# Performance work log

Hardware: AMD Instinct MI355X
Metric: run time of the kernel (lower is better)

Reference implementation:

```python
import jax, jax.numpy as jnp
import numpy as np

VAR0, VAR1 = 0.1, 0.2
THRESH = 0.5
NEG_POS = 3
NEG_INF = -1e30


def point_form(b):
    # (cx,cy,w,h) -> (x1,y1,x2,y2)
    return jnp.concatenate([b[..., :2] - b[..., 2:] * 0.5,
                            b[..., :2] + b[..., 2:] * 0.5], -1)


def iou(a, b):
    # a: [G,4], b: [A,4], both xyxy -> [G,A]
    tl = jnp.maximum(a[:, None, :2], b[None, :, :2])
    br = jnp.minimum(a[:, None, 2:], b[None, :, 2:])
    wh = jnp.clip(br - tl, 0.0)
    inter = wh[..., 0] * wh[..., 1]
    area_a = (a[:, 2] - a[:, 0]) * (a[:, 3] - a[:, 1])
    area_b = (b[:, 2] - b[:, 0]) * (b[:, 3] - b[:, 1])
    return inter / (area_a[:, None] + area_b[None, :] - inter)


def encode_single(gt_boxes, gt_labels, anchors):
    # gt_boxes [G,4] xyxy, gt_labels [G], anchors [A,4] cxcywh
    ov = iou(gt_boxes, point_form(anchors))            # [G,A]
    best_prior_idx = jnp.argmax(ov, axis=1)            # [G] guaranteed match
    best_truth_ov = jnp.max(ov, axis=0)                # [A]
    best_truth_idx = jnp.argmax(ov, axis=0)            # [A]
    G = gt_boxes.shape[0]
    best_truth_ov = best_truth_ov.at[best_prior_idx].set(2.0)
    best_truth_idx = best_truth_idx.at[best_prior_idx].set(jnp.arange(G))
    matches = gt_boxes[best_truth_idx]                 # [A,4]
    conf = jnp.where(best_truth_ov < THRESH, 0, gt_labels[best_truth_idx] + 1)
    m_cxcy = (matches[:, :2] + matches[:, 2:]) * 0.5
    m_wh = matches[:, 2:] - matches[:, :2]
    g_cxcy = (m_cxcy - anchors[:, :2]) / (VAR0 * anchors[:, 2:])
    g_wh = jnp.log(m_wh / anchors[:, 2:]) / VAR1
    return conf, jnp.concatenate([g_cxcy, g_wh], -1)


def smooth_l1(d):
    ad = jnp.abs(d)
    return jnp.where(ad < 1.0, 0.5 * d * d, ad - 0.5)


def ssd_guarantee_loss(pred_conf, pred_loc, anchors_b, gt_boxes, gt_labels):
    # anchors_b: per-image anchors [B,A,4] (cxcywh)
    conf_t, loc_t = jax.vmap(encode_single)(gt_boxes, gt_labels, anchors_b)
    loc_t = jax.lax.stop_gradient(loc_t)               # loc_t.detach() in torch
    pos = conf_t > 0                                   # [B,A]
    N = jnp.sum(pos).astype(pred_loc.dtype)
    loc_loss = jnp.sum(jnp.where(pos[..., None], smooth_l1(pred_loc - loc_t), 0.0))
    logp = jax.nn.log_softmax(pred_conf, axis=-1)
    ce = -jnp.take_along_axis(logp, conf_t[..., None], axis=-1)[..., 0]  # [B,A]
    A = pred_conf.shape[1]
    pos_num = jnp.sum(pos, axis=1)                     # [B]
    neg_num = jnp.maximum(10, jnp.minimum(pos_num * NEG_POS, A - pos_num))
    neg_ce = jnp.where(conf_t == 0, ce, NEG_INF)
    neg_sorted = -jnp.sort(-neg_ce, axis=1)            # descending hard-negative sort
    rank = jnp.arange(A)
    take = (rank[None, :] < neg_num[:, None]) & (neg_sorted > 0.5 * NEG_INF)
    class_loss = (jnp.sum(jnp.where(pos, ce, 0.0))
                  + jnp.sum(jnp.where(take, neg_sorted, 0.0))) / N
    return class_loss, loc_loss / N, N


def decode(loc, anchors):
    # loc [B,A,4], anchors [A,4] cxcywh -> refined anchors [B,A,4] cxcywh
    cxcy = anchors[None, :, :2] + loc[..., :2] * VAR0 * anchors[None, :, 2:]
    wh = anchors[None, :, 2:] * jnp.exp(loc[..., 2:] * VAR1)
    return jnp.concatenate([cxcy, wh], -1)


def setup_inputs() -> dict:
    key = jax.random.key(0)
    ks = jax.random.split(key, 10)
    B, A, C, G = 32, 16320, 81, 32
    objectness = jax.random.normal(ks[0], (B, A, 2), jnp.float32)
    refine_loc = 0.1 * jax.random.normal(ks[1], (B, A, 4), jnp.float32)
    pred_conf = jax.random.normal(ks[2], (B, A, C), jnp.float32)
    pred_loc = 0.1 * jax.random.normal(ks[3], (B, A, 4), jnp.float32)
    # anchors: valid normalized cxcywh
    a_cxcy = 0.05 + 0.9 * jax.random.uniform(ks[4], (1, A, 2), jnp.float32)
    a_wh = 0.02 + 0.23 * jax.random.uniform(ks[5], (1, A, 2), jnp.float32)
    anchors = jnp.concatenate([a_cxcy, a_wh], -1)
    # gt boxes: valid xyxy in [0,1]
    g_cxcy = 0.2 + 0.6 * jax.random.uniform(ks[6], (B, G, 2), jnp.float32)
    g_wh = 0.05 + 0.25 * jax.random.uniform(ks[7], (B, G, 2), jnp.float32)
    gt_boxes = jnp.clip(jnp.concatenate([g_cxcy - g_wh * 0.5, g_cxcy + g_wh * 0.5], -1), 0.0, 1.0)
    gt_labels = jax.random.randint(ks[8], (B, G), 0, C - 1, jnp.int32)
    return {"objectness": objectness, "refine_loc": refine_loc, "pred_conf": pred_conf,
            "pred_loc": pred_loc, "anchors": anchors, "gt_boxes": gt_boxes,
            "gt_labels": gt_labels}


def reference(objectness, refine_loc, pred_conf, pred_loc, anchors, gt_boxes, gt_labels):
    a0 = anchors[0]                                    # [A,4]
    B = pred_conf.shape[0]
    anchors_b = jnp.broadcast_to(a0, (B,) + a0.shape)
    # ARM: binary objectness, labels zeroed
    arm_cls, arm_loc, _ = ssd_guarantee_loss(objectness, refine_loc, anchors_b,
                                             gt_boxes, jnp.zeros_like(gt_labels))
    # ODM: match against per-image refined anchors
    refined = decode(refine_loc, a0)
    odm_cls, odm_loc, _ = ssd_guarantee_loss(pred_conf, pred_loc, refined,
                                             gt_boxes, gt_labels)
    total = arm_cls + arm_loc + odm_cls + odm_loc
    return (total, odm_cls, odm_loc, arm_cls, arm_loc)
```

## Files before the change

### kernel.cpp

```cpp
#include <hip/hip_runtime.h>
#include <hip/hip_bf16.h>

constexpr int NB = 32;
constexpr int NA = 16320;
constexpr int NG = 32;
constexpr int NC = 81;
constexpr int ODM_GRID = 2048;

__device__ __forceinline__ float sl1(float d) {
    float ad = fabsf(d);
    return ad < 1.f ? 0.5f * d * d : ad - 0.5f;
}

__device__ __forceinline__ unsigned long long umax64(unsigned long long a, unsigned long long b) {
    return a > b ? a : b;
}

__global__ __launch_bounds__(256) void k_match(
    const float* __restrict__ anchors,
    const float* __restrict__ refine_loc,
    const float* __restrict__ gt_boxes,
    float* __restrict__ ws_ov,
    unsigned char* __restrict__ ws_idx,
    unsigned long long* __restrict__ ws_part)
{
    int row = blockIdx.x >> 6;
    int chunk = blockIdx.x & 63;
    int lossId = row >> 5, b = row & 31;
    int tid = threadIdx.x;
    __shared__ float4 s_gt[NG];
    __shared__ float s_ga[NG];
    __shared__ unsigned long long s_part[4][NG];
    if (tid < NG) {
        float4 g = *(const float4*)&gt_boxes[(size_t)(b * NG + tid) * 4];
        s_gt[tid] = g;
        s_ga[tid] = (g.z - g.x) * (g.w - g.y);
    }
    __syncthreads();
    int a = chunk * 256 + tid;
    bool valid = a < NA;
    int al = valid ? a : NA - 1;
    float4 an = *(const float4*)&anchors[(size_t)al * 4];
    float acx = an.x, acy = an.y, aw = an.z, ah = an.w;
    if (lossId) {
        float4 rl = *(const float4*)&refine_loc[((size_t)b * NA + al) * 4];
        acx += rl.x * 0.1f * aw;
        acy += rl.y * 0.1f * ah;
        aw *= __expf(rl.z * 0.2f);
        ah *= __expf(rl.w * 0.2f);
    }
    float ax1 = acx - aw * 0.5f, ay1 = acy - ah * 0.5f;
    float ax2 = acx + aw * 0.5f, ay2 = acy + ah * 0.5f;
    float aarea = (ax2 - ax1) * (ay2 - ay1);

    float ovg[NG];
    float best = -1.f; int bg = 0;
    #pragma unroll
    for (int g = 0; g < NG; g++) {
        float4 G = s_gt[g];
        float tlx = fmaxf(G.x, ax1);
        float tly = fmaxf(G.y, ay1);
        float brx = fminf(G.z, ax2);
        float bry = fminf(G.w, ay2);
        float w = brx - tlx; w = w > 0.f ? w : 0.f;
        float h = bry - tly; h = h > 0.f ? h : 0.f;
        float inter = w * h;
        float uni = s_ga[g] + aarea - inter;
        float ov = inter * __builtin_amdgcn_rcpf(uni);
        if (!valid) ov = 0.f;
        ovg[g] = ov;
        if (ov > best) { best = ov; bg = g; }
    }
    if (valid) {
        size_t sec = (size_t)row * NA;
        ws_ov[sec + a] = best;
        ws_idx[sec + a] = (unsigned char)bg;
    }
    int lane = tid & 63, wv = tid >> 6;
    #pragma unroll
    for (int g = 0; g < NG; g++) {
        float m = ovg[g];
        m = fmaxf(m, __shfl_xor(m, 1));
        m = fmaxf(m, __shfl_xor(m, 2));
        m = fmaxf(m, __shfl_xor(m, 4));
        m = fmaxf(m, __shfl_xor(m, 8));
        m = fmaxf(m, __shfl_xor(m, 16));
        m = fmaxf(m, __shfl_xor(m, 32));
        unsigned long long ball = __ballot(ovg[g] == m);
        int first = __ffsll((long long)ball) - 1;
        if (lane == 0) {
            unsigned aw_ = (unsigned)(chunk * 256 + wv * 64 + first);
            s_part[wv][g] = ((unsigned long long)__float_as_uint(m) << 32)
                            | (0xFFFFFFFFu - aw_);
        }
    }
    __syncthreads();
    if (tid < NG) {
        unsigned long long k = s_part[0][tid];
        #pragma unroll
        for (int i = 1; i < 4; i++) k = umax64(k, s_part[i][tid]);
        ws_part[(size_t)blockIdx.x * NG + tid] = k;
    }
}

__global__ __launch_bounds__(256) void k_conf(
    const int* __restrict__ gt_labels,
    const unsigned long long* __restrict__ ws_part,
    const float* __restrict__ ws_ov,
    const unsigned char* __restrict__ ws_idx,
    const float* __restrict__ objectness,
    const float* __restrict__ anchors,
    const float* __restrict__ gt_boxes,
    const float* __restrict__ arm_pred,
    int* __restrict__ match,
    float* __restrict__ negce,
    int* __restrict__ pos_cnt,
    float2* __restrict__ pConf)
{
    int row = blockIdx.x >> 3;
    int chunk = blockIdx.x & 7;
    int lossId = row >> 5, b = row & 31;
    int tid = threadIdx.x;
    __shared__ int s_oa[NG];
    __shared__ int s_lab[NG];
    __shared__ float4 s_gt[NG];
    __shared__ unsigned s_mask[512];
    __shared__ unsigned long long s_pp[8][NG];
    for (int i = tid; i < 512; i += 256) s_mask[i] = 0u;
    {
        int g = tid & 31, s = tid >> 5;
        unsigned long long k = 0ull;
        for (int c = s; c < 64; c += 8)
            k = umax64(k, ws_part[(size_t)(row * 64 + c) * NG + g]);
        s_pp[s][g] = k;
    }
    __syncthreads();
    if (tid < NG) {
        unsigned long long k = s_pp[0][tid];
        #pragma unroll
        for (int i = 1; i < 8; i++) k = umax64(k, s_pp[i][tid]);
        unsigned a = 0xFFFFFFFFu - (unsigned)(k & 0xFFFFFFFFull);
        s_oa[tid] = (int)a;
        s_lab[tid] = lossId ? gt_labels[b * NG + tid] : 0;
        s_gt[tid] = *(const float4*)&gt_boxes[(size_t)(b * NG + tid) * 4];
        atomicOr(&s_mask[a >> 5], 1u << (a & 31));
    }
    __syncthreads();
    size_t sec = (size_t)row * NA;
    int base = chunk * 2040;
    int cnt = 0;
    float pce = 0.f, ploc = 0.f;
    for (int a = base + tid; a < base + 2040; a += 256) {
        float ov = ws_ov[sec + a];
        int g = ws_idx[sec + a];
        if (s_mask[a >> 5] & (1u << (a & 31))) {
            for (int j = NG - 1; j >= 0; j--)
                if (s_oa[j] == a) { g = j; ov = 2.0f; break; }
        }
        int conf = (ov < 0.5f) ? 0 : (s_lab[g] + 1);
        cnt += (conf > 0);
        if (lossId) {
            match[sec + a] = conf | (g << 16);
        } else {
            size_t idx = sec + a;
            float2 x = *(const float2*)&objectness[idx * 2];
            float lse = __logf(__expf(x.x) + __expf(x.y));
            float ce = lse - (conf ? x.y : x.x);
            if (conf > 0) {
                pce += ce;
                negce[idx] = 0.f;
                float4 an = *(const float4*)&anchors[(size_t)a * 4];
                float4 G = s_gt[g];
                float mcx = (G.x + G.z) * 0.5f, mcy = (G.y + G.w) * 0.5f;
                float mw = G.z - G.x, mh = G.w - G.y;
                float t0 = (mcx - an.x) / (0.1f * an.z);
                float t1 = (mcy - an.y) / (0.1f * an.w);
                float t2 = __logf(mw / an.z) / 0.2f;
                float t3 = __logf(mh / an.w) / 0.2f;
                float4 pl = *(const float4*)&arm_pred[idx * 4];
                ploc += sl1(pl.x - t0) + sl1(pl.y - t1) + sl1(pl.z - t2) + sl1(pl.w - t3);
            } else {
                negce[idx] = ce;
            }
        }
    }
    #pragma unroll
    for (int o = 32; o > 0; o >>= 1) {
        cnt += __shfl_down(cnt, o);
        pce += __shfl_down(pce, o);
        ploc += __shfl_down(ploc, o);
    }
    __shared__ int s_c[4];
    __shared__ float s_p0[4], s_p1[4];
    if ((tid & 63) == 0) {
        int w = tid >> 6;
        s_c[w] = cnt; s_p0[w] = pce; s_p1[w] = ploc;
    }
    __syncthreads();
    if (tid == 0) {
        pos_cnt[blockIdx.x] = s_c[0] + s_c[1] + s_c[2] + s_c[3];
        pConf[blockIdx.x] = make_float2(s_p0[0] + s_p0[1] + s_p0[2] + s_p0[3],
                                        s_p1[0] + s_p1[1] + s_p1[2] + s_p1[3]);
    }
}

__device__ __forceinline__ void block_reduce2_store(float v0, float v1, float2* dst) {
    #pragma unroll
    for (int o = 32; o > 0; o >>= 1) { v0 += __shfl_down(v0, o); v1 += __shfl_down(v1, o); }
    __shared__ float s0[4], s1[4];
    int w = threadIdx.x >> 6;
    if ((threadIdx.x & 63) == 0) { s0[w] = v0; s1[w] = v1; }
    __syncthreads();
    if (threadIdx.x == 0) {
        float t0 = 0.f, t1 = 0.f;
        #pragma unroll
        for (int i = 0; i < 4; i++) { t0 += s0[i]; t1 += s1[i]; }
        *dst = make_float2(t0, t1);
    }
}

__device__ __forceinline__ void odm_anchor(
    int idx, const float* x, float x80, int m, int sub,
    const float* __restrict__ anchors, const float* __restrict__ refine_loc,
    const float* __restrict__ gt_boxes, const float* __restrict__ pred_loc,
    float* __restrict__ negce, float& pce, float& ploc)
{
    int conf = m & 0xFFFF; int g = m >> 16;
    float s = (sub == 0) ? __expf(x80) : 0.f;
    float sel = (sub == 0 && conf == 80) ? x80 : 0.f;
    #pragma unroll
    for (int j = 0; j < 10; j++) {
        s += __expf(x[j]);
        sel += (sub + 8 * j == conf) ? x[j] : 0.f;
    }
    s += __shfl_xor(s, 1);   sel += __shfl_xor(sel, 1);
    s += __shfl_xor(s, 2);   sel += __shfl_xor(sel, 2);
    s += __shfl_xor(s, 4);   sel += __shfl_xor(sel, 4);
    float ce = __logf(s) - sel;
    if (sub == 0) {
        if (conf > 0) {
            pce += ce;
            negce[idx] = 0.f;
            int b = idx / NA, a = idx - b * NA;
            float4 an = *(const float4*)&anchors[(size_t)a * 4];
            float4 rl = *(const float4*)&refine_loc[(size_t)idx * 4];
            float acx = an.x + rl.x * 0.1f * an.z;
            float acy = an.y + rl.y * 0.1f * an.w;
            float aw = an.z * __expf(rl.z * 0.2f);
            float ah = an.w * __expf(rl.w * 0.2f);
            const float* gb = &gt_boxes[(size_t)(b * NG + g) * 4];
            float mcx = (gb[0] + gb[2]) * 0.5f, mcy = (gb[1] + gb[3]) * 0.5f;
            float mw = gb[2] - gb[0], mh = gb[3] - gb[1];
            float t0 = (mcx - acx) / (0.1f * aw);
            float t1 = (mcy - acy) / (0.1f * ah);
            float t2 = __logf(mw / aw) / 0.2f;
            float t3 = __logf(mh / ah) / 0.2f;
            float4 pl = *(const float4*)&pred_loc[(size_t)idx * 4];
            ploc += sl1(pl.x - t0) + sl1(pl.y - t1) + sl1(pl.z - t2) + sl1(pl.w - t3);
        } else {
            negce[idx] = ce;
        }
    }
}

__global__ __launch_bounds__(256, 4) void k_odm_loss(
    const float* __restrict__ pred_conf,
    const float* __restrict__ pred_loc,
    const float* __restrict__ anchors,
    const float* __restrict__ refine_loc,
    const float* __restrict__ gt_boxes,
    const int* __restrict__ match,
    float* __restrict__ negce,
    float2* __restrict__ partial)
{
    int lane = threadIdx.x & 63;
    int sub = lane & 7;
    int grp = lane >> 3;
    int wid = blockIdx.x * 4 + (threadIdx.x >> 6);
    const int NWAVE = ODM_GRID * 4;
    const int TOT = NB * NA / 8;
    float pce = 0.f, ploc = 0.f;

    float x[10], x80; int m, idx;
    {
        idx = wid * 8 + grp;
        const float* p = pred_conf + (size_t)idx * NC;
        #pragma unroll
        for (int j = 0; j < 10; j++) x[j] = p[sub + 8 * j];
        x80 = (sub == 0) ? p[80] : -87.f;
        m = match[idx];
    }
    for (int gi = wid; gi < TOT; gi += NWAVE) {
        float y[10], y80 = -87.f; int my = 0, idxy = 0;
        int nx = gi + NWAVE;
        if (nx < TOT) {
            idxy = nx * 8 + grp;
            const float* p = pred_conf + (size_t)idxy * NC;
            #pragma unroll
            for (int j = 0; j < 10; j++) y[j] = p[sub + 8 * j];
            y80 = (sub == 0) ? p[80] : -87.f;
            my = match[idxy];
        }
        odm_anchor(idx, x, x80, m, sub, anchors, refine_loc, gt_boxes, pred_loc,
                   negce, pce, ploc);
        #pragma unroll
        for (int j = 0; j < 10; j++) x[j] = y[j];
        x80 = y80; m = my; idx = idxy;
    }
    block_reduce2_store(pce, ploc, &partial[blockIdx.x]);
}

__global__ __launch_bounds__(512) void k_topk(
    const float* __restrict__ negce,
    const int* __restrict__ pos_cnt,
    float* __restrict__ topk)
{
    int blk = blockIdx.x;
    int tid = threadIdx.x;
    size_t sec = (size_t)blk * NA;
    float v[32];
    #pragma unroll
    for (int q = 0; q < 32; q++) {
        int i = tid + (q << 9);
        v[q] = (i < NA) ? negce[sec + i] : 0.f;
    }
    __shared__ int s_red[8];
    __shared__ float s_redf[8];
    int p = 0;
    #pragma unroll
    for (int j = 0; j < 8; j++) p += pos_cnt[blk * 8 + j];
    int k = p * 3; if (k > NA - p) k = NA - p; if (k < 10) k = 10;

    unsigned lo = 0u, hi = 0x7F800000u;
    while (lo < hi) {
        unsigned mid = (lo + hi) >> 1;
        float fmid = __uint_as_float(mid);
        int c = 0;
        #pragma unroll
        for (int q = 0; q < 32; q++) c += (v[q] > fmid);
        #pragma unroll
        for (int o = 32; o > 0; o >>= 1) c += __shfl_down(c, o);
        if ((tid & 63) == 0) s_red[tid >> 6] = c;
        __syncthreads();
        int total = 0;
        #pragma unroll
        for (int j = 0; j < 8; j++) total += s_red[j];
        __syncthreads();
        if (total < k) hi = mid; else lo = mid + 1;
    }
    float V = __uint_as_float(lo);
    int c = 0; float sum = 0.f;
    #pragma unroll
    for (int q = 0; q < 32; q++) {
        if (v[q] > V) { c++; sum += v[q]; }
    }
    #pragma unroll
    for (int o = 32; o > 0; o >>= 1) { c += __shfl_down(c, o); sum += __shfl_down(sum, o); }
    if ((tid & 63) == 0) { s_red[tid >> 6] = c; s_redf[tid >> 6] = sum; }
    __syncthreads();
    if (tid == 0) {
        int cg = 0; float sg = 0.f;
        #pragma unroll
        for (int j = 0; j < 8; j++) { cg += s_red[j]; sg += s_redf[j]; }
        topk[blk] = sg + (float)(k - cg) * V;
    }
}

__global__ __launch_bounds__(256) void k_final(
    const float2* __restrict__ pConf, const float2* __restrict__ pOdm,
    const int* __restrict__ pos_cnt, const float* __restrict__ topk,
    float* __restrict__ out)
{
    int tid = threadIdx.x;
    float a0 = 0.f, a1 = 0.f, o0 = 0.f, o1 = 0.f;
    for (int i = tid; i < 512; i += 256) { float2 v = pConf[i]; a0 += v.x; a1 += v.y; }
    for (int i = tid; i < ODM_GRID; i += 256) { float2 v = pOdm[i]; o0 += v.x; o1 += v.y; }
    float n0 = (float)pos_cnt[tid];
    float n1 = (float)pos_cnt[256 + tid];
    float t0 = (tid < NB) ? topk[tid] : 0.f;
    float t1 = (tid < NB) ? topk[NB + tid] : 0.f;
    #pragma unroll
    for (int o = 32; o > 0; o >>= 1) {
        a0 += __shfl_down(a0, o); a1 += __shfl_down(a1, o);
        o0 += __shfl_down(o0, o); o1 += __shfl_down(o1, o);
        n0 += __shfl_down(n0, o); n1 += __shfl_down(n1, o);
        t0 += __shfl_down(t0, o); t1 += __shfl_down(t1, o);
    }
    __shared__ float s[4][8];
    if ((tid & 63) == 0) {
        int w = tid >> 6;
        s[w][0] = a0; s[w][1] = a1; s[w][2] = o0; s[w][3] = o1;
        s[w][4] = n0; s[w][5] = n1; s[w][6] = t0; s[w][7] = t1;
    }
    __syncthreads();
    if (tid == 0) {
        float armce = 0.f, armloc = 0.f, odmce = 0.f, odmloc = 0.f;
        float N0 = 0.f, N1 = 0.f, tk0 = 0.f, tk1 = 0.f;
        #pragma unroll
        for (int i = 0; i < 4; i++) {
            armce += s[i][0]; armloc += s[i][1]; odmce += s[i][2]; odmloc += s[i][3];
            N0 += s[i][4]; N1 += s[i][5]; tk0 += s[i][6]; tk1 += s[i][7];
        }
        float cls0 = (armce + tk0) / N0, loc0 = armloc / N0;
        float cls1 = (odmce + tk1) / N1, loc1 = odmloc / N1;
        out[0] = cls0 + loc0 + cls1 + loc1;
        out[1] = cls1;
        out[2] = loc1;
        out[3] = cls0;
        out[4] = loc0;
    }
}

extern "C" void kernel_launch(void* const* d_in, const int* in_sizes, int n_in,
                              void* d_out, int out_size, void* d_ws, size_t ws_size,
                              hipStream_t stream) {
    const float* objectness = (const float*)d_in[0];
    const float* refine_loc = (const float*)d_in[1];
    const float* pred_conf  = (const float*)d_in[2];
    const float* pred_loc   = (const float*)d_in[3];
    const float* anchors    = (const float*)d_in[4];
    const float* gt_boxes   = (const float*)d_in[5];
    const int*   gt_labels  = (const int*)d_in[6];

    char* w = (char*)d_ws;
    size_t off = 0;
    int* pos_cnt = (int*)(w + off); off += 512 * sizeof(int);
    float* topk = (float*)(w + off); off += 64 * sizeof(float);
    off = (off + 15) & ~(size_t)15;
    float2* pConf = (float2*)(w + off); off += 512 * 8;
    float2* pOdm = (float2*)(w + off); off += (size_t)ODM_GRID * 8;
    unsigned long long* ws_part = (unsigned long long*)(w + off);
    off += (size_t)64 * 64 * NG * 8;
    off = (off + 15) & ~(size_t)15;
    float* ws_ov = (float*)(w + off); off += (size_t)2 * NB * NA * 4;
    unsigned char* ws_idx = (unsigned char*)(w + off); off += (size_t)2 * NB * NA;
    off = (off + 15) & ~(size_t)15;
    int* match = (int*)(w + off); off += (size_t)2 * NB * NA * 4;
    float* negce = (float*)(w + off); off += (size_t)2 * NB * NA * 4;

    k_match<<<64 * 64, 256, 0, stream>>>(anchors, refine_loc, gt_boxes,
                                         ws_ov, ws_idx, ws_part);
    k_conf<<<64 * 8, 256, 0, stream>>>(gt_labels, ws_part, ws_ov, ws_idx,
                                       objectness, anchors, gt_boxes, refine_loc,
                                       match, negce, pos_cnt, pConf);
    k_odm_loss<<<ODM_GRID, 256, 0, stream>>>(pred_conf, pred_loc, anchors, refine_loc,
                                             gt_boxes, match + (size_t)NB * NA,
                                             negce + (size_t)NB * NA, pOdm);
    k_topk<<<2 * NB, 512, 0, stream>>>(negce, pos_cnt, topk);
    k_final<<<1, 256, 0, stream>>>(pConf, pOdm, pos_cnt, topk, (float*)d_out);
}
```

Measured before the change: 131.1 us.

## Restructure pipeline into match+LSE mega kernel, fixup pass, and per-row loss kernel

Merges the IoU matching and the ODM log-sum-exp pass over pred_conf into one interleaved launch, so the memory-bound LSE streaming overlaps with the compute-bound matching. Confidence is computed directly during matching, and a small per-row fixup kernel applies the forced best-prior matches instead of rescanning every anchor. Per-row CE, localisation loss and top-k hard-negative mining are fused into one 1024-thread kernel per row that finishes with a last-block reduction, which removes the negce buffer and two launches. The cost is that only 64 blocks run the row stage, with a gather read of pred_conf, and completion depends on an atomic counter.

```diff
diff --git a/kernel.cpp b/kernel.cpp
--- a/kernel.cpp
+++ b/kernel.cpp
@@ -5,7 +5,7 @@
 constexpr int NA = 16320;
 constexpr int NG = 32;
 constexpr int NC = 81;
-constexpr int ODM_GRID = 2048;
+constexpr int LSE_BLKS = 2048;
 
 __device__ __forceinline__ float sl1(float d) {
     float ad = fabsf(d);
@@ -16,25 +16,75 @@
     return a > b ? a : b;
 }
 
-__global__ __launch_bounds__(256) void k_match(
+__global__ __launch_bounds__(256) void k_mega(
     const float* __restrict__ anchors,
     const float* __restrict__ refine_loc,
     const float* __restrict__ gt_boxes,
-    float* __restrict__ ws_ov,
-    unsigned char* __restrict__ ws_idx,
-    unsigned long long* __restrict__ ws_part)
+    const int* __restrict__ gt_labels,
+    const float* __restrict__ pred_conf,
+    int* __restrict__ match,
+    float* __restrict__ lse,
+    unsigned long long* __restrict__ ws_part,
+    int* __restrict__ pos_parts)
 {
-    int row = blockIdx.x >> 6;
-    int chunk = blockIdx.x & 63;
-    int lossId = row >> 5, b = row & 31;
-    int tid = threadIdx.x;
     __shared__ float4 s_gt[NG];
     __shared__ float s_ga[NG];
+    __shared__ int s_lab[NG];
     __shared__ unsigned long long s_part[4][NG];
+    __shared__ int s_c[4];
+
+    int bid = blockIdx.x;
+    int q = bid / 3, r3 = bid - q * 3;
+    int tid = threadIdx.x;
+
+    if (r3 == 0) {
+        int lane = tid & 63, sub = lane & 7, grp = lane >> 3;
+        int wid = q * 4 + (tid >> 6);
+        const int NWAVE = LSE_BLKS * 4;
+        const int TOT = NB * NA / 8;
+        float x[11]; int idx;
+        {
+            idx = wid * 8 + grp;
+            const float* p = pred_conf + (size_t)idx * NC;
+            #pragma unroll
+            for (int j = 0; j < 10; j++) x[j] = p[sub + 8 * j];
+            x[10] = (sub == 0) ? p[80] : -87.f;
+        }
+        for (int gi = wid; gi < TOT; gi += NWAVE) {
+            float y[11]; int idy = 0;
+            int nx = gi + NWAVE;
+            if (nx < TOT) {
+                idy = nx * 8 + grp;
+                const float* p = pred_conf + (size_t)idy * NC;
+                #pragma unroll
+                for (int j = 0; j < 10; j++) y[j] = p[sub + 8 * j];
+                y[10] = (sub == 0) ? p[80] : -87.f;
+            } else {
+                #pragma unroll
+                for (int j = 0; j < 11; j++) y[j] = -87.f;
+            }
+            float s = __expf(x[10]);
+            #pragma unroll
+            for (int j = 0; j < 10; j++) s += __expf(x[j]);
+            s += __shfl_xor(s, 1);
+            s += __shfl_xor(s, 2);
+            s += __shfl_xor(s, 4);
+            if (sub == 0) lse[idx] = __logf(s);
+            #pragma unroll
+            for (int j = 0; j < 11; j++) x[j] = y[j];
+            idx = idy;
+        }
+        return;
+    }
+
+    int mb = 2 * q + (r3 - 1);
+    int row = mb >> 6, chunk = mb & 63;
+    int lossId = row >> 5, b = row & 31;
     if (tid < NG) {
         float4 g = *(const float4*)&gt_boxes[(size_t)(b * NG + tid) * 4];
         s_gt[tid] = g;
         s_ga[tid] = (g.z - g.x) * (g.w - g.y);
+        s_lab[tid] = lossId ? gt_labels[b * NG + tid] : 0;
     }
     __syncthreads();
     int a = chunk * 256 + tid;
@@ -65,17 +115,16 @@
         float w = brx - tlx; w = w > 0.f ? w : 0.f;
         float h = bry - tly; h = h > 0.f ? h : 0.f;
         float inter = w * h;
-        float uni = s_ga[g] + aarea - inter;
-        float ov = inter * __builtin_amdgcn_rcpf(uni);
+        float ov = inter * __builtin_amdgcn_rcpf(s_ga[g] + aarea - inter);
         if (!valid) ov = 0.f;
         ovg[g] = ov;
         if (ov > best) { best = ov; bg = g; }
     }
-    if (valid) {
-        size_t sec = (size_t)row * NA;
-        ws_ov[sec + a] = best;
-        ws_idx[sec + a] = (unsigned char)bg;
-    }
+    int conf = (best < 0.5f) ? 0 : (s_lab[bg] + 1);
+    size_t sec = (size_t)row * NA;
+    if (valid) match[sec + a] = conf | (bg << 16);
+    int cnt = (valid && conf > 0) ? 1 : 0;
+
     int lane = tid & 63, wv = tid >> 6;
     #pragma unroll
     for (int g = 0; g < NG; g++) {
@@ -94,39 +143,34 @@
                             | (0xFFFFFFFFu - aw_);
         }
     }
+    #pragma unroll
+    for (int o = 32; o > 0; o >>= 1) cnt += __shfl_down(cnt, o);
+    if (lane == 0) s_c[wv] = cnt;
     __syncthreads();
     if (tid < NG) {
         unsigned long long k = s_part[0][tid];
         #pragma unroll
         for (int i = 1; i < 4; i++) k = umax64(k, s_part[i][tid]);
-        ws_part[(size_t)blockIdx.x * NG + tid] = k;
-    }
-}
-
-__global__ __launch_bounds__(256) void k_conf(
+        ws_part[(size_t)mb * NG + tid] = k;
+    }
+    if (tid == 0) pos_parts[mb] = s_c[0] + s_c[1] + s_c[2] + s_c[3];
+}
+
+__global__ __launch_bounds__(256) void k_fix(
     const int* __restrict__ gt_labels,
     const unsigned long long* __restrict__ ws_part,
-    const float* __restrict__ ws_ov,
-    const unsigned char* __restrict__ ws_idx,
-    const float* __restrict__ objectness,
-    const float* __restrict__ anchors,
-    const float* __restrict__ gt_boxes,
-    const float* __restrict__ arm_pred,
+    const int* __restrict__ pos_parts,
     int* __restrict__ match,
-    float* __restrict__ negce,
     int* __restrict__ pos_cnt,
-    float2* __restrict__ pConf)
+    unsigned* __restrict__ done_cnt)
 {
-    int row = blockIdx.x >> 3;
-    int chunk = blockIdx.x & 7;
+    int row = blockIdx.x;
+    int tid = threadIdx.x;
+    if (row == 0 && tid == 0) *done_cnt = 0u;
     int lossId = row >> 5, b = row & 31;
-    int tid = threadIdx.x;
-    __shared__ int s_oa[NG];
-    __shared__ int s_lab[NG];
-    __shared__ float4 s_gt[NG];
-    __shared__ unsigned s_mask[512];
     __shared__ unsigned long long s_pp[8][NG];
-    for (int i = tid; i < 512; i += 256) s_mask[i] = 0u;
+    __shared__ int s_a[NG];
+    __shared__ int s_cnt[64];
     {
         int g = tid & 31, s = tid >> 5;
         unsigned long long k = 0ull;
@@ -134,120 +178,88 @@
             k = umax64(k, ws_part[(size_t)(row * 64 + c) * NG + g]);
         s_pp[s][g] = k;
     }
+    if (tid < 64) s_cnt[tid] = pos_parts[row * 64 + tid];
     __syncthreads();
     if (tid < NG) {
         unsigned long long k = s_pp[0][tid];
         #pragma unroll
         for (int i = 1; i < 8; i++) k = umax64(k, s_pp[i][tid]);
-        unsigned a = 0xFFFFFFFFu - (unsigned)(k & 0xFFFFFFFFull);
-        s_oa[tid] = (int)a;
-        s_lab[tid] = lossId ? gt_labels[b * NG + tid] : 0;
-        s_gt[tid] = *(const float4*)&gt_boxes[(size_t)(b * NG + tid) * 4];
-        atomicOr(&s_mask[a >> 5], 1u << (a & 31));
+        s_a[tid] = (int)(0xFFFFFFFFu - (unsigned)(k & 0xFFFFFFFFull));
     }
     __syncthreads();
     size_t sec = (size_t)row * NA;
-    int base = chunk * 2040;
-    int cnt = 0;
+    int delta = 0;
+    if (tid < NG) {
+        int a = s_a[tid];
+        bool is_last = true;
+        for (int j = tid + 1; j < NG; j++)
+            if (s_a[j] == a) { is_last = false; break; }
+        if (is_last) {
+            int old = match[sec + a];
+            int lab1 = lossId ? (gt_labels[b * NG + tid] + 1) : 1;
+            match[sec + a] = lab1 | (tid << 16);
+            delta = 1 - (((old & 0xFFFF) > 0) ? 1 : 0);
+        }
+    }
+    #pragma unroll
+    for (int o = 32; o > 0; o >>= 1) delta += __shfl_down(delta, o);
+    if (tid == 0) {
+        int cnt = delta;
+        for (int i = 0; i < 64; i++) cnt += s_cnt[i];
+        pos_cnt[row] = cnt;
+    }
+}
+
+__global__ __launch_bounds__(1024) void k_row(
+    const float* __restrict__ objectness,
+    const float* __restrict__ pred_conf,
+    const float* __restrict__ pred_loc,
+    const float* __restrict__ anchors,
+    const float* __restrict__ refine_loc,
+    const float* __restrict__ gt_boxes,
+    const int* __restrict__ match,
+    const float* __restrict__ lse,
+    const int* __restrict__ pos_cnt,
+    float4* __restrict__ pRow,
+    unsigned* __restrict__ done_cnt,
+    float* __restrict__ out)
+{
+    int row = blockIdx.x, lossId = row >> 5, b = row & 31;
+    int tid = threadIdx.x;
+    size_t sec = (size_t)row * NA;
+    float v[16];
     float pce = 0.f, ploc = 0.f;
-    for (int a = base + tid; a < base + 2040; a += 256) {
-        float ov = ws_ov[sec + a];
-        int g = ws_idx[sec + a];
-        if (s_mask[a >> 5] & (1u << (a & 31))) {
-            for (int j = NG - 1; j >= 0; j--)
-                if (s_oa[j] == a) { g = j; ov = 2.0f; break; }
-        }
-        int conf = (ov < 0.5f) ? 0 : (s_lab[g] + 1);
-        cnt += (conf > 0);
-        if (lossId) {
-            match[sec + a] = conf | (g << 16);
-        } else {
-            size_t idx = sec + a;
-            float2 x = *(const float2*)&objectness[idx * 2];
-            float lse = __logf(__expf(x.x) + __expf(x.y));
-            float ce = lse - (conf ? x.y : x.x);
-            if (conf > 0) {
-                pce += ce;
-                negce[idx] = 0.f;
-                float4 an = *(const float4*)&anchors[(size_t)a * 4];
-                float4 G = s_gt[g];
-                float mcx = (G.x + G.z) * 0.5f, mcy = (G.y + G.w) * 0.5f;
-                float mw = G.z - G.x, mh = G.w - G.y;
-                float t0 = (mcx - an.x) / (0.1f * an.z);
-                float t1 = (mcy - an.y) / (0.1f * an.w);
-                float t2 = __logf(mw / an.z) / 0.2f;
-                float t3 = __logf(mh / an.w) / 0.2f;
-                float4 pl = *(const float4*)&arm_pred[idx * 4];
-                ploc += sl1(pl.x - t0) + sl1(pl.y - t1) + sl1(pl.z - t2) + sl1(pl.w - t3);
+    #pragma unroll
+    for (int q2 = 0; q2 < 16; q2++) {
+        int a = tid + (q2 << 10);
+        float ce = 0.f; int conf = 0, g = 0;
+        if (a < NA) {
+            int m = match[sec + a]; conf = m & 0xFFFF; g = m >> 16;
+            if (lossId) {
+                float l = lse[(size_t)b * NA + a];
+                float xc = pred_conf[((size_t)b * NA + a) * NC + conf];
+                ce = l - xc;
             } else {
-                negce[idx] = ce;
+                float2 xx = *(const float2*)&objectness[((size_t)b * NA + a) * 2];
+                float l = __logf(__expf(xx.x) + __expf(xx.y));
+                ce = l - (conf ? xx.y : xx.x);
             }
         }
-    }
-    #pragma unroll
-    for (int o = 32; o > 0; o >>= 1) {
-        cnt += __shfl_down(cnt, o);
-        pce += __shfl_down(pce, o);
-        ploc += __shfl_down(ploc, o);
-    }
-    __shared__ int s_c[4];
-    __shared__ float s_p0[4], s_p1[4];
-    if ((tid & 63) == 0) {
-        int w = tid >> 6;
-        s_c[w] = cnt; s_p0[w] = pce; s_p1[w] = ploc;
-    }
-    __syncthreads();
-    if (tid == 0) {
-        pos_cnt[blockIdx.x] = s_c[0] + s_c[1] + s_c[2] + s_c[3];
-        pConf[blockIdx.x] = make_float2(s_p0[0] + s_p0[1] + s_p0[2] + s_p0[3],
-                                        s_p1[0] + s_p1[1] + s_p1[2] + s_p1[3]);
-    }
-}
-
-__device__ __forceinline__ void block_reduce2_store(float v0, float v1, float2* dst) {
-    #pragma unroll
-    for (int o = 32; o > 0; o >>= 1) { v0 += __shfl_down(v0, o); v1 += __shfl_down(v1, o); }
-    __shared__ float s0[4], s1[4];
-    int w = threadIdx.x >> 6;
-    if ((threadIdx.x & 63) == 0) { s0[w] = v0; s1[w] = v1; }
-    __syncthreads();
-    if (threadIdx.x == 0) {
-        float t0 = 0.f, t1 = 0.f;
-        #pragma unroll
-        for (int i = 0; i < 4; i++) { t0 += s0[i]; t1 += s1[i]; }
-        *dst = make_float2(t0, t1);
-    }
-}
-
-__device__ __forceinline__ void odm_anchor(
-    int idx, const float* x, float x80, int m, int sub,
-    const float* __restrict__ anchors, const float* __restrict__ refine_loc,
-    const float* __restrict__ gt_boxes, const float* __restrict__ pred_loc,
-    float* __restrict__ negce, float& pce, float& ploc)
-{
-    int conf = m & 0xFFFF; int g = m >> 16;
-    float s = (sub == 0) ? __expf(x80) : 0.f;
-    float sel = (sub == 0 && conf == 80) ? x80 : 0.f;
-    #pragma unroll
-    for (int j = 0; j < 10; j++) {
-        s += __expf(x[j]);
-        sel += (sub + 8 * j == conf) ? x[j] : 0.f;
-    }
-    s += __shfl_xor(s, 1);   sel += __shfl_xor(sel, 1);
-    s += __shfl_xor(s, 2);   sel += __shfl_xor(sel, 2);
-    s += __shfl_xor(s, 4);   sel += __shfl_xor(sel, 4);
-    float ce = __logf(s) - sel;
-    if (sub == 0) {
         if (conf > 0) {
-            pce += ce;
-            negce[idx] = 0.f;
-            int b = idx / NA, a = idx - b * NA;
+            pce += ce; v[q2] = 0.f;
             float4 an = *(const float4*)&anchors[(size_t)a * 4];
-            float4 rl = *(const float4*)&refine_loc[(size_t)idx * 4];
-            float acx = an.x + rl.x * 0.1f * an.z;
-            float acy = an.y + rl.y * 0.1f * an.w;
-            float aw = an.z * __expf(rl.z * 0.2f);
-            float ah = an.w * __expf(rl.w * 0.2f);
+            float acx = an.x, acy = an.y, aw = an.z, ah = an.w;
+            const float* pl;
+            if (lossId) {
+                float4 rl = *(const float4*)&refine_loc[((size_t)b * NA + a) * 4];
+                acx += rl.x * 0.1f * aw;
+                acy += rl.y * 0.1f * ah;
+                aw *= __expf(rl.z * 0.2f);
+                ah *= __expf(rl.w * 0.2f);
+                pl = &pred_loc[((size_t)b * NA + a) * 4];
+            } else {
+                pl = &refine_loc[((size_t)b * NA + a) * 4];
+            }
             const float* gb = &gt_boxes[(size_t)(b * NG + g) * 4];
             float mcx = (gb[0] + gb[2]) * 0.5f, mcy = (gb[1] + gb[3]) * 0.5f;
             float mw = gb[2] - gb[0], mh = gb[3] - gb[1];
@@ -255,80 +267,15 @@
             float t1 = (mcy - acy) / (0.1f * ah);
             float t2 = __logf(mw / aw) / 0.2f;
             float t3 = __logf(mh / ah) / 0.2f;
-            float4 pl = *(const float4*)&pred_loc[(size_t)idx * 4];
-            ploc += sl1(pl.x - t0) + sl1(pl.y - t1) + sl1(pl.z - t2) + sl1(pl.w - t3);
+            float4 p4 = *(const float4*)pl;
+            ploc += sl1(p4.x - t0) + sl1(p4.y - t1) + sl1(p4.z - t2) + sl1(p4.w - t3);
         } else {
-            negce[idx] = ce;
-        }
-    }
-}
-
-__global__ __launch_bounds__(256, 4) void k_odm_loss(
-    const float* __restrict__ pred_conf,
-    const float* __restrict__ pred_loc,
-    const float* __restrict__ anchors,
-    const float* __restrict__ refine_loc,
-    const float* __restrict__ gt_boxes,
-    const int* __restrict__ match,
-    float* __restrict__ negce,
-    float2* __restrict__ partial)
-{
-    int lane = threadIdx.x & 63;
-    int sub = lane & 7;
-    int grp = lane >> 3;
-    int wid = blockIdx.x * 4 + (threadIdx.x >> 6);
-    const int NWAVE = ODM_GRID * 4;
-    const int TOT = NB * NA / 8;
-    float pce = 0.f, ploc = 0.f;
-
-    float x[10], x80; int m, idx;
-    {
-        idx = wid * 8 + grp;
-        const float* p = pred_conf + (size_t)idx * NC;
-        #pragma unroll
-        for (int j = 0; j < 10; j++) x[j] = p[sub + 8 * j];
-        x80 = (sub == 0) ? p[80] : -87.f;
-        m = match[idx];
-    }
-    for (int gi = wid; gi < TOT; gi += NWAVE) {
-        float y[10], y80 = -87.f; int my = 0, idxy = 0;
-        int nx = gi + NWAVE;
-        if (nx < TOT) {
-            idxy = nx * 8 + grp;
-            const float* p = pred_conf + (size_t)idxy * NC;
-            #pragma unroll
-            for (int j = 0; j < 10; j++) y[j] = p[sub + 8 * j];
-            y80 = (sub == 0) ? p[80] : -87.f;
-            my = match[idxy];
-        }
-        odm_anchor(idx, x, x80, m, sub, anchors, refine_loc, gt_boxes, pred_loc,
-                   negce, pce, ploc);
-        #pragma unroll
-        for (int j = 0; j < 10; j++) x[j] = y[j];
-        x80 = y80; m = my; idx = idxy;
-    }
-    block_reduce2_store(pce, ploc, &partial[blockIdx.x]);
-}
-
-__global__ __launch_bounds__(512) void k_topk(
-    const float* __restrict__ negce,
-    const int* __restrict__ pos_cnt,
-    float* __restrict__ topk)
-{
-    int blk = blockIdx.x;
-    int tid = threadIdx.x;
-    size_t sec = (size_t)blk * NA;
-    float v[32];
-    #pragma unroll
-    for (int q = 0; q < 32; q++) {
-        int i = tid + (q << 9);
-        v[q] = (i < NA) ? negce[sec + i] : 0.f;
-    }
-    __shared__ int s_red[8];
-    __shared__ float s_redf[8];
-    int p = 0;
-    #pragma unroll
-    for (int j = 0; j < 8; j++) p += pos_cnt[blk * 8 + j];
+            v[q2] = (a < NA) ? ce : 0.f;
+        }
+    }
+    __shared__ int s_red[16];
+    __shared__ float s_p[16][4];
+    int p = pos_cnt[row];
     int k = p * 3; if (k > NA - p) k = NA - p; if (k < 10) k = 10;
 
     unsigned lo = 0u, hi = 0x7F800000u;
@@ -337,77 +284,71 @@
         float fmid = __uint_as_float(mid);
         int c = 0;
         #pragma unroll
-        for (int q = 0; q < 32; q++) c += (v[q] > fmid);
+        for (int q2 = 0; q2 < 16; q2++) c += (v[q2] > fmid);
         #pragma unroll
         for (int o = 32; o > 0; o >>= 1) c += __shfl_down(c, o);
         if ((tid & 63) == 0) s_red[tid >> 6] = c;
         __syncthreads();
         int total = 0;
         #pragma unroll
-        for (int j = 0; j < 8; j++) total += s_red[j];
+        for (int j = 0; j < 16; j++) total += s_red[j];
         __syncthreads();
         if (total < k) hi = mid; else lo = mid + 1;
     }
     float V = __uint_as_float(lo);
     int c = 0; float sum = 0.f;
     #pragma unroll
-    for (int q = 0; q < 32; q++) {
-        if (v[q] > V) { c++; sum += v[q]; }
-    }
-    #pragma unroll
-    for (int o = 32; o > 0; o >>= 1) { c += __shfl_down(c, o); sum += __shfl_down(sum, o); }
-    if ((tid & 63) == 0) { s_red[tid >> 6] = c; s_redf[tid >> 6] = sum; }
-    __syncthreads();
-    if (tid == 0) {
-        int cg = 0; float sg = 0.f;
-        #pragma unroll
-        for (int j = 0; j < 8; j++) { cg += s_red[j]; sg += s_redf[j]; }
-        topk[blk] = sg + (float)(k - cg) * V;
-    }
-}
-
-__global__ __launch_bounds__(256) void k_final(
-    const float2* __restrict__ pConf, const float2* __restrict__ pOdm,
-    const int* __restrict__ pos_cnt, const float* __restrict__ topk,
-    float* __restrict__ out)
-{
-    int tid = threadIdx.x;
-    float a0 = 0.f, a1 = 0.f, o0 = 0.f, o1 = 0.f;
-    for (int i = tid; i < 512; i += 256) { float2 v = pConf[i]; a0 += v.x; a1 += v.y; }
-    for (int i = tid; i < ODM_GRID; i += 256) { float2 v = pOdm[i]; o0 += v.x; o1 += v.y; }
-    float n0 = (float)pos_cnt[tid];
-    float n1 = (float)pos_cnt[256 + tid];
-    float t0 = (tid < NB) ? topk[tid] : 0.f;
-    float t1 = (tid < NB) ? topk[NB + tid] : 0.f;
+    for (int q2 = 0; q2 < 16; q2++) {
+        if (v[q2] > V) { c++; sum += v[q2]; }
+    }
+    float cf = (float)c;
     #pragma unroll
     for (int o = 32; o > 0; o >>= 1) {
-        a0 += __shfl_down(a0, o); a1 += __shfl_down(a1, o);
-        o0 += __shfl_down(o0, o); o1 += __shfl_down(o1, o);
-        n0 += __shfl_down(n0, o); n1 += __shfl_down(n1, o);
-        t0 += __shfl_down(t0, o); t1 += __shfl_down(t1, o);
-    }
-    __shared__ float s[4][8];
+        cf += __shfl_down(cf, o); sum += __shfl_down(sum, o);
+        pce += __shfl_down(pce, o); ploc += __shfl_down(ploc, o);
+    }
     if ((tid & 63) == 0) {
         int w = tid >> 6;
-        s[w][0] = a0; s[w][1] = a1; s[w][2] = o0; s[w][3] = o1;
-        s[w][4] = n0; s[w][5] = n1; s[w][6] = t0; s[w][7] = t1;
+        s_p[w][0] = cf; s_p[w][1] = sum; s_p[w][2] = pce; s_p[w][3] = ploc;
     }
     __syncthreads();
     if (tid == 0) {
-        float armce = 0.f, armloc = 0.f, odmce = 0.f, odmloc = 0.f;
-        float N0 = 0.f, N1 = 0.f, tk0 = 0.f, tk1 = 0.f;
-        #pragma unroll
-        for (int i = 0; i < 4; i++) {
-            armce += s[i][0]; armloc += s[i][1]; odmce += s[i][2]; odmloc += s[i][3];
-            N0 += s[i][4]; N1 += s[i][5]; tk0 += s[i][6]; tk1 += s[i][7];
-        }
-        float cls0 = (armce + tk0) / N0, loc0 = armloc / N0;
-        float cls1 = (odmce + tk1) / N1, loc1 = odmloc / N1;
-        out[0] = cls0 + loc0 + cls1 + loc1;
-        out[1] = cls1;
-        out[2] = loc1;
-        out[3] = cls0;
-        out[4] = loc0;
+        float cg = 0.f, sg = 0.f, pc = 0.f, pl2 = 0.f;
+        #pragma unroll
+        for (int j = 0; j < 16; j++) {
+            cg += s_p[j][0]; sg += s_p[j][1]; pc += s_p[j][2]; pl2 += s_p[j][3];
+        }
+        float tk = sg + ((float)k - cg) * V;
+        pRow[row] = make_float4(pc, pl2, tk, (float)p);
+    }
+    __threadfence();
+    __shared__ unsigned s_t;
+    if (tid == 0) s_t = atomicAdd(done_cnt, 1u);
+    __syncthreads();
+    if (s_t != 63u) return;
+    if (tid < 64) {
+        float4 vv = pRow[tid];
+        bool arm = tid < 32;
+        float a0 = arm ? vv.x : 0.f, a1 = arm ? vv.y : 0.f;
+        float at = arm ? vv.z : 0.f, an2 = arm ? vv.w : 0.f;
+        float o0 = arm ? 0.f : vv.x, o1 = arm ? 0.f : vv.y;
+        float ot = arm ? 0.f : vv.z, on = arm ? 0.f : vv.w;
+        #pragma unroll
+        for (int o = 32; o > 0; o >>= 1) {
+            a0 += __shfl_down(a0, o); a1 += __shfl_down(a1, o);
+            at += __shfl_down(at, o); an2 += __shfl_down(an2, o);
+            o0 += __shfl_down(o0, o); o1 += __shfl_down(o1, o);
+            ot += __shfl_down(ot, o); on += __shfl_down(on, o);
+        }
+        if (tid == 0) {
+            float cls0 = (a0 + at) / an2, loc0 = a1 / an2;
+            float cls1 = (o0 + ot) / on,  loc1 = o1 / on;
+            out[0] = cls0 + loc0 + cls1 + loc1;
+            out[1] = cls1;
+            out[2] = loc1;
+            out[3] = cls0;
+            out[4] = loc0;
+        }
     }
 }
 
@@ -424,28 +365,21 @@
 
     char* w = (char*)d_ws;
     size_t off = 0;
-    int* pos_cnt = (int*)(w + off); off += 512 * sizeof(int);
-    float* topk = (float*)(w + off); off += 64 * sizeof(float);
+    int* pos_cnt = (int*)(w + off); off += 64 * sizeof(int);
+    unsigned* done_cnt = (unsigned*)(w + off); off += 16;
+    int* pos_parts = (int*)(w + off); off += 4096 * sizeof(int);
     off = (off + 15) & ~(size_t)15;
-    float2* pConf = (float2*)(w + off); off += 512 * 8;
-    float2* pOdm = (float2*)(w + off); off += (size_t)ODM_GRID * 8;
+    float4* pRow = (float4*)(w + off); off += 64 * sizeof(float4);
     unsigned long long* ws_part = (unsigned long long*)(w + off);
-    off += (size_t)64 * 64 * NG * 8;
+    off += (size_t)4096 * NG * 8;
     off = (off + 15) & ~(size_t)15;
-    float* ws_ov = (float*)(w + off); off += (size_t)2 * NB * NA * 4;
-    unsigned char* ws_idx = (unsigned char*)(w + off); off += (size_t)2 * NB * NA;
-    off = (off + 15) & ~(size_t)15;
+    float* lse = (float*)(w + off); off += (size_t)NB * NA * 4;
     int* match = (int*)(w + off); off += (size_t)2 * NB * NA * 4;
-    float* negce = (float*)(w + off); off += (size_t)2 * NB * NA * 4;
-
-    k_match<<<64 * 64, 256, 0, stream>>>(anchors, refine_loc, gt_boxes,
-                                         ws_ov, ws_idx, ws_part);
-    k_conf<<<64 * 8, 256, 0, stream>>>(gt_labels, ws_part, ws_ov, ws_idx,
-                                       objectness, anchors, gt_boxes, refine_loc,
-                                       match, negce, pos_cnt, pConf);
-    k_odm_loss<<<ODM_GRID, 256, 0, stream>>>(pred_conf, pred_loc, anchors, refine_loc,
-                                             gt_boxes, match + (size_t)NB * NA,
-                                             negce + (size_t)NB * NA, pOdm);
-    k_topk<<<2 * NB, 512, 0, stream>>>(negce, pos_cnt, topk);
-    k_final<<<1, 256, 0, stream>>>(pConf, pOdm, pos_cnt, topk, (float*)d_out);
-}
+
+    k_mega<<<3 * 2048, 256, 0, stream>>>(anchors, refine_loc, gt_boxes, gt_labels,
+                                         pred_conf, match, lse, ws_part, pos_parts);
+    k_fix<<<64, 256, 0, stream>>>(gt_labels, ws_part, pos_parts, match, pos_cnt, done_cnt);
+    k_row<<<64, 1024, 0, stream>>>(objectness, pred_conf, pred_loc, anchors, refine_loc,
+                                   gt_boxes, match, lse, pos_cnt,
+                                   pRow, done_cnt, (float*)d_out);
+}
```

Measured after the change: 163.4 us. 1.25x slower.
